# Kernel optimization log

Hardware: AMD Instinct MI355X
Metric: run time of the kernel (lower is better)

The kernel has to match this reference:

```python
import jax, jax.numpy as jnp
import numpy as np

H_SIZE = 1024
N_HEADS = 16
D_K = H_SIZE // N_HEADS


def setup_inputs() -> dict:
    key = jax.random.key(0)
    ks = jax.random.split(key, 12)
    s = 1.0 / np.sqrt(H_SIZE)
    inp = {
        "x": jax.random.normal(ks[0], (2, 2048, H_SIZE), dtype=jnp.float32),
        "Wq": jax.random.uniform(ks[1], (H_SIZE, H_SIZE), minval=-s, maxval=s),
        "bq": jax.random.uniform(ks[2], (H_SIZE,), minval=-s, maxval=s),
        "Wk": jax.random.uniform(ks[3], (H_SIZE, H_SIZE), minval=-s, maxval=s),
        "bk": jax.random.uniform(ks[4], (H_SIZE,), minval=-s, maxval=s),
        "Wv": jax.random.uniform(ks[5], (H_SIZE, H_SIZE), minval=-s, maxval=s),
        "bv": jax.random.uniform(ks[6], (H_SIZE,), minval=-s, maxval=s),
        "Wo": jax.random.uniform(ks[7], (H_SIZE, H_SIZE), minval=-s, maxval=s),
        "bo": jax.random.uniform(ks[8], (H_SIZE,), minval=-s, maxval=s),
        "ln_gamma": jnp.ones((H_SIZE,), dtype=jnp.float32),
        "ln_beta": jnp.zeros((H_SIZE,), dtype=jnp.float32),
    }
    return inp


def reference(x, Wq, bq, Wk, bk, Wv, bv, Wo, bo, ln_gamma, ln_beta):
    B, L, H = x.shape
    residual = x
    # QKV projections -> [B, n_heads, L, d_k]
    def proj(W, b):
        return (x @ W.T + b).reshape(B, L, N_HEADS, D_K).transpose(0, 2, 1, 3)
    q = proj(Wq, bq)
    k = proj(Wk, bk)
    v = proj(Wv, bv)
    # scaled dot-product attention (dropout = identity in eval mode)
    scores = jnp.einsum("bhqd,bhkd->bhqk", q, k) / jnp.sqrt(jnp.float32(D_K))
    attn = jax.nn.softmax(scores, axis=-1)
    out = jnp.einsum("bhqk,bhkd->bhqd", attn, v)
    out = out.transpose(0, 2, 1, 3).reshape(B, L, H)
    out = out @ Wo.T + bo
    # residual + LayerNorm
    y = out + residual
    mu = jnp.mean(y, axis=-1, keepdims=True)
    var = jnp.var(y, axis=-1, keepdims=True)
    y = (y - mu) / jnp.sqrt(var + 1e-5) * ln_gamma + ln_beta
    return y
```

## Files before the change

kernel.cpp:

```cpp
#include <hip/hip_runtime.h>

#define H_SIZE 1024
#define N_HEADS 16
#define D_K 64
#define SEQ 2048
#define BATCH 2
#define M_TOT 4096

typedef __bf16 __attribute__((ext_vector_type(8))) bf16_8;
typedef float __attribute__((ext_vector_type(4))) f32x4;
typedef float __attribute__((ext_vector_type(16))) f32x16;
typedef int __attribute__((ext_vector_type(4))) int4v;

__device__ __forceinline__ ushort f2bf(float f) {
    unsigned int u = __float_as_uint(f);
    unsigned int r = (u + 0x7FFFu + ((u >> 16) & 1u)) >> 16;
    return (ushort)r;
}

__device__ __forceinline__ unsigned int cvtpk(float lo, float hi) {
    unsigned int r;
    asm("v_cvt_pk_bf16_f32 %0, %1, %2" : "=v"(r) : "v"(lo), "v"(hi));
    return r;
}

__device__ __forceinline__ void gld16(void* lds, const void* g) {
    __builtin_amdgcn_global_load_lds(
        (const __attribute__((address_space(1))) unsigned int*)g,
        (__attribute__((address_space(3))) unsigned int*)lds, 16, 0, 0);
}

__global__ __launch_bounds__(256) void cast_all_kernel(
    const float* __restrict__ x, const float* __restrict__ wq, const float* __restrict__ wk,
    const float* __restrict__ wv, const float* __restrict__ wo,
    ushort* __restrict__ xb, ushort* __restrict__ wqb, ushort* __restrict__ wkb,
    ushort* __restrict__ wvb, ushort* __restrict__ wob) {
    int i = blockIdx.x * 256 + threadIdx.x;
    const float* src;
    ushort* dst;
    int off;
    if (i < 1048576) {
        src = x; dst = xb; off = i;
    } else {
        int j = i - 1048576;
        int w = j >> 18;
        off = j & 262143;
        src = (w == 0) ? wq : (w == 1) ? wk : (w == 2) ? wv : wo;
        dst = (w == 0) ? wqb : (w == 1) ? wkb : (w == 2) ? wvb : wob;
    }
    float4 v = ((const float4*)src)[off];
    ushort4 o;
    o.x = f2bf(v.x); o.y = f2bf(v.y); o.z = f2bf(v.z); o.w = f2bf(v.w);
    ((ushort4*)dst)[off] = o;
}

__global__ __launch_bounds__(256) void gemm_qkv(
    const ushort* __restrict__ A, const ushort* __restrict__ wq,
    const ushort* __restrict__ wk, const ushort* __restrict__ wv,
    const float* __restrict__ bq, const float* __restrict__ bk, const float* __restrict__ bv,
    ushort* __restrict__ Qb, ushort* __restrict__ Kb, ushort* __restrict__ Vtb) {
    constexpr int BK = 64, LDST = 72;
    __shared__ ushort As[128 * LDST];
    __shared__ ushort Bs[128 * LDST];
    const int tid = threadIdx.x;
    const int lane = tid & 63, wid = tid >> 6;
    const int wr = wid >> 1, wc = wid & 1;
    const int hi = lane >> 4, lo = lane & 15;
    const int bm0 = blockIdx.x * 128;
    const int t3 = blockIdx.y >> 3;
    const int bn0 = (blockIdx.y & 7) * 128;
    const ushort* Bw = (t3 == 0) ? wq : (t3 == 1) ? wk : wv;
    const float* bias = (t3 == 0) ? bq : (t3 == 1) ? bk : bv;
    ushort* outp = (t3 == 0) ? Qb : (t3 == 1) ? Kb : Vtb;

    f32x4 acc[4][4] = {};

    const int r = tid >> 1, seg = (tid & 1) * 32;
    const ushort* ga = A + (size_t)(bm0 + r) * H_SIZE + seg;
    const ushort* gb = Bw + (size_t)(bn0 + r) * H_SIZE + seg;
    ushort* sa = As + r * LDST + seg;
    ushort* sb = Bs + r * LDST + seg;

    for (int kt = 0; kt < H_SIZE; kt += BK) {
        int4v a0 = *(const int4v*)(ga);
        int4v a1 = *(const int4v*)(ga + 8);
        int4v a2 = *(const int4v*)(ga + 16);
        int4v a3 = *(const int4v*)(ga + 24);
        int4v b0 = *(const int4v*)(gb);
        int4v b1 = *(const int4v*)(gb + 8);
        int4v b2 = *(const int4v*)(gb + 16);
        int4v b3 = *(const int4v*)(gb + 24);
        ga += BK; gb += BK;
        __syncthreads();
        *(int4v*)(sa) = a0; *(int4v*)(sa + 8) = a1;
        *(int4v*)(sa + 16) = a2; *(int4v*)(sa + 24) = a3;
        *(int4v*)(sb) = b0; *(int4v*)(sb + 8) = b1;
        *(int4v*)(sb + 16) = b2; *(int4v*)(sb + 24) = b3;
        __syncthreads();
#pragma unroll
        for (int kk = 0; kk < BK; kk += 32) {
            bf16_8 af[4], bfr[4];
            const ushort* pa = As + (wr * 64 + lo) * LDST + kk + hi * 8;
            const ushort* pb = Bs + (wc * 64 + lo) * LDST + kk + hi * 8;
#pragma unroll
            for (int i = 0; i < 4; i++) af[i] = *(const bf16_8*)(pa + i * 16 * LDST);
#pragma unroll
            for (int i = 0; i < 4; i++) bfr[i] = *(const bf16_8*)(pb + i * 16 * LDST);
#pragma unroll
            for (int mi = 0; mi < 4; mi++)
#pragma unroll
                for (int ni = 0; ni < 4; ni++)
                    acc[mi][ni] = __builtin_amdgcn_mfma_f32_16x16x32_bf16(
                        af[mi], bfr[ni], acc[mi][ni], 0, 0, 0);
        }
    }

#pragma unroll
    for (int mi = 0; mi < 4; mi++) {
#pragma unroll
        for (int ni = 0; ni < 4; ni++) {
            const int row0 = bm0 + wr * 64 + mi * 16 + hi * 4;
            const int col = bn0 + wc * 64 + ni * 16 + lo;
            const float bv = bias[col];
            const int h = col >> 6, dk = col & 63;
#pragma unroll
            for (int rr = 0; rr < 4; rr++) {
                const int m = row0 + rr;
                const int b = m >> 11, l = m & 2047;
                float val = acc[mi][ni][rr] + bv;
                if (t3 == 0) {
                    outp[((size_t)(b * N_HEADS + h) * SEQ + l) * D_K + dk] = f2bf(val * 0.125f);
                } else if (t3 == 1) {
                    int dks = (((dk >> 3) ^ (l & 7)) << 3) | (dk & 7);
                    outp[((size_t)(b * N_HEADS + h) * SEQ + l) * D_K + dks] = f2bf(val);
                } else {
                    int lsw = (l & ~63) | ((((l >> 3) & 7) ^ (dk & 7)) << 3) | (l & 7);
                    outp[((size_t)(b * N_HEADS + h) * D_K + dk) * SEQ + lsw] = f2bf(val);
                }
            }
        }
    }
}

__global__ __launch_bounds__(256) void gemm_o(const ushort* __restrict__ A,
                                              const ushort* __restrict__ Bw,
                                              const float* __restrict__ bias,
                                              const float* __restrict__ resid,
                                              float* __restrict__ outp) {
    constexpr int BK = 64, LDST = 72;
    __shared__ ushort As[128 * LDST];
    __shared__ ushort Bs[64 * LDST];
    const int tid = threadIdx.x;
    const int lane = tid & 63, wid = tid >> 6;
    const int wr = wid >> 1, wc = wid & 1;
    const int hi = lane >> 4, lo = lane & 15;
    const int bm0 = blockIdx.x * 128, bn0 = blockIdx.y * 64;

    f32x4 acc[4][2] = {};

    const int ra = tid >> 1, sega = (tid & 1) * 32;
    const int rb = tid >> 2, segb = (tid & 3) * 16;
    const ushort* ga = A + (size_t)(bm0 + ra) * H_SIZE + sega;
    const ushort* gb = Bw + (size_t)(bn0 + rb) * H_SIZE + segb;
    ushort* sa = As + ra * LDST + sega;
    ushort* sb = Bs + rb * LDST + segb;

    for (int kt = 0; kt < H_SIZE; kt += BK) {
        int4v a0 = *(const int4v*)(ga);
        int4v a1 = *(const int4v*)(ga + 8);
        int4v a2 = *(const int4v*)(ga + 16);
        int4v a3 = *(const int4v*)(ga + 24);
        int4v b0 = *(const int4v*)(gb);
        int4v b1 = *(const int4v*)(gb + 8);
        ga += BK; gb += BK;
        __syncthreads();
        *(int4v*)(sa) = a0; *(int4v*)(sa + 8) = a1;
        *(int4v*)(sa + 16) = a2; *(int4v*)(sa + 24) = a3;
        *(int4v*)(sb) = b0; *(int4v*)(sb + 8) = b1;
        __syncthreads();
#pragma unroll
        for (int kk = 0; kk < BK; kk += 32) {
            bf16_8 af[4], bfr[2];
            const ushort* pa = As + (wr * 64 + lo) * LDST + kk + hi * 8;
            const ushort* pb = Bs + (wc * 32 + lo) * LDST + kk + hi * 8;
#pragma unroll
            for (int i = 0; i < 4; i++) af[i] = *(const bf16_8*)(pa + i * 16 * LDST);
#pragma unroll
            for (int i = 0; i < 2; i++) bfr[i] = *(const bf16_8*)(pb + i * 16 * LDST);
#pragma unroll
            for (int mi = 0; mi < 4; mi++)
#pragma unroll
                for (int ni = 0; ni < 2; ni++)
                    acc[mi][ni] = __builtin_amdgcn_mfma_f32_16x16x32_bf16(
                        af[mi], bfr[ni], acc[mi][ni], 0, 0, 0);
        }
    }

#pragma unroll
    for (int mi = 0; mi < 4; mi++) {
#pragma unroll
        for (int ni = 0; ni < 2; ni++) {
            const int row0 = bm0 + wr * 64 + mi * 16 + hi * 4;
            const int col = bn0 + wc * 32 + ni * 16 + lo;
            const float bv = bias[col];
#pragma unroll
            for (int rr = 0; rr < 4; rr++) {
                const int m = row0 + rr;
                outp[(size_t)m * H_SIZE + col] =
                    acc[mi][ni][rr] + bv + resid[(size_t)m * H_SIZE + col];
            }
        }
    }
}

__global__ __launch_bounds__(256) void attn_kernel(const ushort* __restrict__ Q,
                                                   const ushort* __restrict__ Ksw,
                                                   const ushort* __restrict__ Vsw,
                                                   ushort* __restrict__ Out) {
    __shared__ ushort Ks[2][64 * 64];
    __shared__ ushort Vs[2][64 * 64];
    __shared__ float lsum_lds[4][32];
    const int lane = threadIdx.x & 63, wid = threadIdx.x >> 6;
    const int h32 = lane >> 5, q32 = lane & 31;
    const int bh = blockIdx.y;
    const int q0w = blockIdx.x * 128 + wid * 32;
    const ushort* Qh = Q + (size_t)bh * SEQ * D_K;
    const ushort* Kp = Ksw + (size_t)bh * SEQ * D_K;
    const ushort* Vp = Vsw + (size_t)bh * D_K * SEQ;

    bf16_8 qf[4];
#pragma unroll
    for (int tt = 0; tt < 4; tt++)
        qf[tt] = *(const bf16_8*)(Qh + (size_t)(q0w + q32) * D_K + tt * 16 + h32 * 8);

    f32x16 oacc0 = {}, oacc1 = {};
    float ls = 0.f;

    const int koff = wid * 2048 + lane * 16;
    const int vrow = wid * 16 + (lane >> 3);
    const int vseg = (lane & 7) * 16;

#define STAGE(bb, kt)                                                             \
    {                                                                             \
        const char* kg = (const char*)(Kp + (size_t)(kt) * D_K);                  \
        char* kl = (char*)&Ks[bb][0];                                             \
        gld16(kl + koff, kg + koff);                                              \
        gld16(kl + koff + 1024, kg + koff + 1024);                                \
        char* vl = (char*)&Vs[bb][0];                                             \
        gld16(vl + vrow * 128 + vseg,                                             \
              (const char*)(Vp + (size_t)vrow * SEQ + (kt)) + vseg);              \
        gld16(vl + (vrow + 8) * 128 + vseg,                                       \
              (const char*)(Vp + (size_t)(vrow + 8) * SEQ + (kt)) + vseg);        \
    }

    STAGE(0, 0);
    __syncthreads();
    int buf = 0;
    for (int t = 0; t < SEQ / 64; t++) {
        if (t + 1 < SEQ / 64) STAGE(buf ^ 1, (t + 1) * 64);
        const ushort* kb = &Ks[buf][0];
        const ushort* vb = &Vs[buf][0];
#pragma unroll
        for (int kh = 0; kh < 2; kh++) {
            f32x16 st = {};
            const int krow = kh * 32 + q32;
#pragma unroll
            for (int tt = 0; tt < 4; tt++) {
                int sg = ((2 * tt + h32) ^ (krow & 7));
                bf16_8 kf = *(const bf16_8*)(kb + krow * 64 + sg * 8);
                st = __builtin_amdgcn_mfma_f32_32x32x16_bf16(kf, qf[tt], st, 0, 0, 0);
            }
            float p[16];
#pragma unroll
            for (int rr = 0; rr < 16; rr++) p[rr] = __expf(st[rr]);
            float partial = 0.f;
#pragma unroll
            for (int rr = 0; rr < 16; rr++) partial += p[rr];
            ls += partial + __shfl_xor(partial, 32);

            union { unsigned int w[4]; bf16_8 v; } pf0, pf1;
#pragma unroll
            for (int i = 0; i < 2; i++) {
                unsigned int a = cvtpk(p[2 * i], p[2 * i + 1]);
                unsigned int b = cvtpk(p[4 + 2 * i], p[4 + 2 * i + 1]);
                asm volatile("v_permlane32_swap_b32 %0, %1" : "+v"(a), "+v"(b));
                pf0.w[i] = a; pf0.w[2 + i] = b;
                unsigned int c = cvtpk(p[8 + 2 * i], p[8 + 2 * i + 1]);
                unsigned int d = cvtpk(p[12 + 2 * i], p[12 + 2 * i + 1]);
                asm volatile("v_permlane32_swap_b32 %0, %1" : "+v"(c), "+v"(d));
                pf1.w[i] = c; pf1.w[2 + i] = d;
            }

            {
                const int vr0 = q32;
                int sg0 = ((4 * kh + h32) ^ (vr0 & 7));
                int sg1 = ((4 * kh + 2 + h32) ^ (vr0 & 7));
                bf16_8 vf0 = *(const bf16_8*)(vb + vr0 * 64 + sg0 * 8);
                bf16_8 vf1 = *(const bf16_8*)(vb + vr0 * 64 + sg1 * 8);
                oacc0 = __builtin_amdgcn_mfma_f32_32x32x16_bf16(pf0.v, vf0, oacc0, 0, 0, 0);
                oacc0 = __builtin_amdgcn_mfma_f32_32x32x16_bf16(pf1.v, vf1, oacc0, 0, 0, 0);
            }
            {
                const int vr1 = 32 + q32;
                int sg0 = ((4 * kh + h32) ^ (vr1 & 7));
                int sg1 = ((4 * kh + 2 + h32) ^ (vr1 & 7));
                bf16_8 vf0 = *(const bf16_8*)(vb + vr1 * 64 + sg0 * 8);
                bf16_8 vf1 = *(const bf16_8*)(vb + vr1 * 64 + sg1 * 8);
                oacc1 = __builtin_amdgcn_mfma_f32_32x32x16_bf16(pf0.v, vf0, oacc1, 0, 0, 0);
                oacc1 = __builtin_amdgcn_mfma_f32_32x32x16_bf16(pf1.v, vf1, oacc1, 0, 0, 0);
            }
        }
        __syncthreads();
        buf ^= 1;
    }
#undef STAGE

    if (lane < 32) lsum_lds[wid][q32] = 1.0f / ls;
    const int b = bh >> 4, h = bh & 15;
#pragma unroll
    for (int rr = 0; rr < 16; rr++) {
        const int qloc = (rr & 3) + 8 * (rr >> 2) + 4 * h32;
        const float inv = lsum_lds[wid][qloc];
        const int l = q0w + qloc;
        ushort* orow = Out + ((size_t)(b * SEQ + l)) * H_SIZE + h * 64;
        orow[q32] = f2bf(oacc0[rr] * inv);
        orow[32 + q32] = f2bf(oacc1[rr] * inv);
    }
}

__global__ __launch_bounds__(256) void ln_kernel(float* __restrict__ y,
                                                 const float* __restrict__ gamma,
                                                 const float* __restrict__ beta) {
    const int row = blockIdx.x;
    float4* p = (float4*)(y + (size_t)row * H_SIZE);
    float4 v = p[threadIdx.x];
    float s = v.x + v.y + v.z + v.w;
    float s2 = v.x * v.x + v.y * v.y + v.z * v.z + v.w * v.w;
#pragma unroll
    for (int off = 1; off < 64; off <<= 1) {
        s += __shfl_xor(s, off);
        s2 += __shfl_xor(s2, off);
    }
    __shared__ float ss[4], ss2[4];
    const int wid = threadIdx.x >> 6, lane = threadIdx.x & 63;
    if (lane == 0) { ss[wid] = s; ss2[wid] = s2; }
    __syncthreads();
    s = ss[0] + ss[1] + ss[2] + ss[3];
    s2 = ss2[0] + ss2[1] + ss2[2] + ss2[3];
    const float mean = s * (1.0f / H_SIZE);
    const float var = s2 * (1.0f / H_SIZE) - mean * mean;
    const float rstd = rsqrtf(var + 1e-5f);
    const float4 g = ((const float4*)gamma)[threadIdx.x];
    const float4 bt = ((const float4*)beta)[threadIdx.x];
    float4 o;
    o.x = (v.x - mean) * rstd * g.x + bt.x;
    o.y = (v.y - mean) * rstd * g.y + bt.y;
    o.z = (v.z - mean) * rstd * g.z + bt.z;
    o.w = (v.w - mean) * rstd * g.w + bt.w;
    p[threadIdx.x] = o;
}

extern "C" void kernel_launch(void* const* d_in, const int* in_sizes, int n_in,
                              void* d_out, int out_size, void* d_ws, size_t ws_size,
                              hipStream_t stream) {
    const float* x = (const float*)d_in[0];
    const float* Wq = (const float*)d_in[1];
    const float* bq = (const float*)d_in[2];
    const float* Wk = (const float*)d_in[3];
    const float* bk = (const float*)d_in[4];
    const float* Wv = (const float*)d_in[5];
    const float* bv = (const float*)d_in[6];
    const float* Wo = (const float*)d_in[7];
    const float* bo = (const float*)d_in[8];
    const float* gamma = (const float*)d_in[9];
    const float* beta = (const float*)d_in[10];

    char* ws = (char*)d_ws;
    ushort* xb  = (ushort*)(ws);
    ushort* wqb = (ushort*)(ws + (8u << 20));
    ushort* wkb = (ushort*)(ws + (10u << 20));
    ushort* wvb = (ushort*)(ws + (12u << 20));
    ushort* wob = (ushort*)(ws + (14u << 20));
    ushort* Qb  = (ushort*)(ws + (16u << 20));
    ushort* Kb  = (ushort*)(ws + (24u << 20));
    ushort* Vtb = (ushort*)(ws + (32u << 20));
    ushort* Ao  = (ushort*)(ws + (40u << 20));

    cast_all_kernel<<<8192, 256, 0, stream>>>(x, Wq, Wk, Wv, Wo, xb, wqb, wkb, wvb, wob);

    dim3 gq(M_TOT / 128, 24);
    gemm_qkv<<<gq, 256, 0, stream>>>(xb, wqb, wkb, wvb, bq, bk, bv, Qb, Kb, Vtb);

    dim3 g2(SEQ / 128, BATCH * N_HEADS);
    attn_kernel<<<g2, 256, 0, stream>>>(Qb, Kb, Vtb, Ao);

    dim3 go(M_TOT / 128, H_SIZE / 64);
    gemm_o<<<go, 256, 0, stream>>>(Ao, wob, bo, x, (float*)d_out);

    ln_kernel<<<M_TOT, 256, 0, stream>>>((float*)d_out, gamma, beta);
}
```

Measured before the change: 141.8 us.

## Double-buffer LDS in QKV and output GEMMs and vectorize V-transpose stores

Both projection GEMMs switch from single-buffered BK=64 tiles with two barriers per step to double-buffered BK=32 tiles. The next tile's global loads are issued before the MFMAs on the current tile, and only one barrier is needed per step. The V output, written transposed, now packs the four consecutive rows of each accumulator into a single ushort4 store instead of four scalar stores. The cost is twice as many loop iterations with less MFMA work each, which may leave less compute to hide latency between barriers.

```diff
diff --git a/kernel.cpp b/kernel.cpp
--- a/kernel.cpp
+++ b/kernel.cpp
@@ -59,9 +59,9 @@
     const ushort* __restrict__ wk, const ushort* __restrict__ wv,
     const float* __restrict__ bq, const float* __restrict__ bk, const float* __restrict__ bv,
     ushort* __restrict__ Qb, ushort* __restrict__ Kb, ushort* __restrict__ Vtb) {
-    constexpr int BK = 64, LDST = 72;
-    __shared__ ushort As[128 * LDST];
-    __shared__ ushort Bs[128 * LDST];
+    constexpr int LDST = 40;
+    __shared__ ushort As[2][128 * LDST];
+    __shared__ ushort Bs[2][128 * LDST];
     const int tid = threadIdx.x;
     const int lane = tid & 63, wid = tid >> 6;
     const int wr = wid >> 1, wc = wid & 1;
@@ -71,49 +71,59 @@
     const int bn0 = (blockIdx.y & 7) * 128;
     const ushort* Bw = (t3 == 0) ? wq : (t3 == 1) ? wk : wv;
     const float* bias = (t3 == 0) ? bq : (t3 == 1) ? bk : bv;
-    ushort* outp = (t3 == 0) ? Qb : (t3 == 1) ? Kb : Vtb;
 
     f32x4 acc[4][4] = {};
 
-    const int r = tid >> 1, seg = (tid & 1) * 32;
-    const ushort* ga = A + (size_t)(bm0 + r) * H_SIZE + seg;
-    const ushort* gb = Bw + (size_t)(bn0 + r) * H_SIZE + seg;
-    ushort* sa = As + r * LDST + seg;
-    ushort* sb = Bs + r * LDST + seg;
-
-    for (int kt = 0; kt < H_SIZE; kt += BK) {
-        int4v a0 = *(const int4v*)(ga);
-        int4v a1 = *(const int4v*)(ga + 8);
-        int4v a2 = *(const int4v*)(ga + 16);
-        int4v a3 = *(const int4v*)(ga + 24);
-        int4v b0 = *(const int4v*)(gb);
-        int4v b1 = *(const int4v*)(gb + 8);
-        int4v b2 = *(const int4v*)(gb + 16);
-        int4v b3 = *(const int4v*)(gb + 24);
-        ga += BK; gb += BK;
-        __syncthreads();
-        *(int4v*)(sa) = a0; *(int4v*)(sa + 8) = a1;
-        *(int4v*)(sa + 16) = a2; *(int4v*)(sa + 24) = a3;
-        *(int4v*)(sb) = b0; *(int4v*)(sb + 8) = b1;
-        *(int4v*)(sb + 16) = b2; *(int4v*)(sb + 24) = b3;
-        __syncthreads();
-#pragma unroll
-        for (int kk = 0; kk < BK; kk += 32) {
-            bf16_8 af[4], bfr[4];
-            const ushort* pa = As + (wr * 64 + lo) * LDST + kk + hi * 8;
-            const ushort* pb = Bs + (wc * 64 + lo) * LDST + kk + hi * 8;
+    const int r = tid >> 1, c0 = (tid & 1) * 16;
+    const ushort* ga = A + (size_t)(bm0 + r) * H_SIZE + c0;
+    const ushort* gb = Bw + (size_t)(bn0 + r) * H_SIZE + c0;
+
+    int4v a0, a1, b0, b1;
+#define LOADR(kt)                                  \
+    {                                              \
+        a0 = *(const int4v*)(ga + (kt));           \
+        a1 = *(const int4v*)(ga + (kt) + 8);       \
+        b0 = *(const int4v*)(gb + (kt));           \
+        b1 = *(const int4v*)(gb + (kt) + 8);       \
+    }
+#define STORER(bb)                                 \
+    {                                              \
+        ushort* sa = &As[bb][r * LDST + c0];       \
+        *(int4v*)sa = a0; *(int4v*)(sa + 8) = a1;  \
+        ushort* sb = &Bs[bb][r * LDST + c0];       \
+        *(int4v*)sb = b0; *(int4v*)(sb + 8) = b1;  \
+    }
+
+    LOADR(0);
+    STORER(0);
+    __syncthreads();
+    int cur = 0;
+    constexpr int NT = H_SIZE / 32;
+    for (int t = 0; t < NT; t++) {
+        if (t + 1 < NT) LOADR((t + 1) * 32);
+        {
+            bf16_8 af[4], bfv[4];
+            const ushort* pa = &As[cur][(wr * 64 + lo) * LDST + hi * 8];
+            const ushort* pb = &Bs[cur][(wc * 64 + lo) * LDST + hi * 8];
 #pragma unroll
             for (int i = 0; i < 4; i++) af[i] = *(const bf16_8*)(pa + i * 16 * LDST);
 #pragma unroll
-            for (int i = 0; i < 4; i++) bfr[i] = *(const bf16_8*)(pb + i * 16 * LDST);
+            for (int i = 0; i < 4; i++) bfv[i] = *(const bf16_8*)(pb + i * 16 * LDST);
 #pragma unroll
             for (int mi = 0; mi < 4; mi++)
 #pragma unroll
                 for (int ni = 0; ni < 4; ni++)
                     acc[mi][ni] = __builtin_amdgcn_mfma_f32_16x16x32_bf16(
-                        af[mi], bfr[ni], acc[mi][ni], 0, 0, 0);
-        }
-    }
+                        af[mi], bfv[ni], acc[mi][ni], 0, 0, 0);
+        }
+        if (t + 1 < NT) {
+            STORER(cur ^ 1);
+            __syncthreads();
+        }
+        cur ^= 1;
+    }
+#undef LOADR
+#undef STORER
 
 #pragma unroll
     for (int mi = 0; mi < 4; mi++) {
@@ -123,19 +133,27 @@
             const int col = bn0 + wc * 64 + ni * 16 + lo;
             const float bv = bias[col];
             const int h = col >> 6, dk = col & 63;
-#pragma unroll
-            for (int rr = 0; rr < 4; rr++) {
-                const int m = row0 + rr;
-                const int b = m >> 11, l = m & 2047;
-                float val = acc[mi][ni][rr] + bv;
-                if (t3 == 0) {
-                    outp[((size_t)(b * N_HEADS + h) * SEQ + l) * D_K + dk] = f2bf(val * 0.125f);
-                } else if (t3 == 1) {
-                    int dks = (((dk >> 3) ^ (l & 7)) << 3) | (dk & 7);
-                    outp[((size_t)(b * N_HEADS + h) * SEQ + l) * D_K + dks] = f2bf(val);
-                } else {
-                    int lsw = (l & ~63) | ((((l >> 3) & 7) ^ (dk & 7)) << 3) | (l & 7);
-                    outp[((size_t)(b * N_HEADS + h) * D_K + dk) * SEQ + lsw] = f2bf(val);
+            if (t3 == 2) {
+                const int b = row0 >> 11, l0 = row0 & 2047;
+                const int lsw0 = (l0 & ~63) | ((((l0 >> 3) & 7) ^ (dk & 7)) << 3) | (l0 & 7);
+                ushort4 o;
+                o.x = f2bf(acc[mi][ni][0] + bv);
+                o.y = f2bf(acc[mi][ni][1] + bv);
+                o.z = f2bf(acc[mi][ni][2] + bv);
+                o.w = f2bf(acc[mi][ni][3] + bv);
+                *(ushort4*)&Vtb[((size_t)(b * N_HEADS + h) * D_K + dk) * SEQ + lsw0] = o;
+            } else {
+#pragma unroll
+                for (int rr = 0; rr < 4; rr++) {
+                    const int m = row0 + rr;
+                    const int b = m >> 11, l = m & 2047;
+                    float val = acc[mi][ni][rr] + bv;
+                    if (t3 == 0) {
+                        Qb[((size_t)(b * N_HEADS + h) * SEQ + l) * D_K + dk] = f2bf(val * 0.125f);
+                    } else {
+                        int dks = (((dk >> 3) ^ (l & 7)) << 3) | (dk & 7);
+                        Kb[((size_t)(b * N_HEADS + h) * SEQ + l) * D_K + dks] = f2bf(val);
+                    }
                 }
             }
         }
@@ -147,9 +165,9 @@
                                               const float* __restrict__ bias,
                                               const float* __restrict__ resid,
                                               float* __restrict__ outp) {
-    constexpr int BK = 64, LDST = 72;
-    __shared__ ushort As[128 * LDST];
-    __shared__ ushort Bs[64 * LDST];
+    constexpr int LDST = 40;
+    __shared__ ushort As[2][128 * LDST];
+    __shared__ ushort Bs[2][64 * LDST];
     const int tid = threadIdx.x;
     const int lane = tid & 63, wid = tid >> 6;
     const int wr = wid >> 1, wc = wid & 1;
@@ -158,43 +176,55 @@
 
     f32x4 acc[4][2] = {};
 
-    const int ra = tid >> 1, sega = (tid & 1) * 32;
-    const int rb = tid >> 2, segb = (tid & 3) * 16;
-    const ushort* ga = A + (size_t)(bm0 + ra) * H_SIZE + sega;
-    const ushort* gb = Bw + (size_t)(bn0 + rb) * H_SIZE + segb;
-    ushort* sa = As + ra * LDST + sega;
-    ushort* sb = Bs + rb * LDST + segb;
-
-    for (int kt = 0; kt < H_SIZE; kt += BK) {
-        int4v a0 = *(const int4v*)(ga);
-        int4v a1 = *(const int4v*)(ga + 8);
-        int4v a2 = *(const int4v*)(ga + 16);
-        int4v a3 = *(const int4v*)(ga + 24);
-        int4v b0 = *(const int4v*)(gb);
-        int4v b1 = *(const int4v*)(gb + 8);
-        ga += BK; gb += BK;
-        __syncthreads();
-        *(int4v*)(sa) = a0; *(int4v*)(sa + 8) = a1;
-        *(int4v*)(sa + 16) = a2; *(int4v*)(sa + 24) = a3;
-        *(int4v*)(sb) = b0; *(int4v*)(sb + 8) = b1;
-        __syncthreads();
-#pragma unroll
-        for (int kk = 0; kk < BK; kk += 32) {
-            bf16_8 af[4], bfr[2];
-            const ushort* pa = As + (wr * 64 + lo) * LDST + kk + hi * 8;
-            const ushort* pb = Bs + (wc * 32 + lo) * LDST + kk + hi * 8;
+    const int ra = tid >> 1, ca0 = (tid & 1) * 16;
+    const int rb = tid >> 2, cb0 = (tid & 3) * 8;
+    const ushort* ga = A + (size_t)(bm0 + ra) * H_SIZE + ca0;
+    const ushort* gb = Bw + (size_t)(bn0 + rb) * H_SIZE + cb0;
+
+    int4v a0, a1, b0;
+#define LOADR(kt)                                  \
+    {                                              \
+        a0 = *(const int4v*)(ga + (kt));           \
+        a1 = *(const int4v*)(ga + (kt) + 8);       \
+        b0 = *(const int4v*)(gb + (kt));           \
+    }
+#define STORER(bb)                                 \
+    {                                              \
+        ushort* sa = &As[bb][ra * LDST + ca0];     \
+        *(int4v*)sa = a0; *(int4v*)(sa + 8) = a1;  \
+        *(int4v*)&Bs[bb][rb * LDST + cb0] = b0;    \
+    }
+
+    LOADR(0);
+    STORER(0);
+    __syncthreads();
+    int cur = 0;
+    constexpr int NT = H_SIZE / 32;
+    for (int t = 0; t < NT; t++) {
+        if (t + 1 < NT) LOADR((t + 1) * 32);
+        {
+            bf16_8 af[4], bfv[2];
+            const ushort* pa = &As[cur][(wr * 64 + lo) * LDST + hi * 8];
+            const ushort* pb = &Bs[cur][(wc * 32 + lo) * LDST + hi * 8];
 #pragma unroll
             for (int i = 0; i < 4; i++) af[i] = *(const bf16_8*)(pa + i * 16 * LDST);
 #pragma unroll
-            for (int i = 0; i < 2; i++) bfr[i] = *(const bf16_8*)(pb + i * 16 * LDST);
+            for (int i = 0; i < 2; i++) bfv[i] = *(const bf16_8*)(pb + i * 16 * LDST);
 #pragma unroll
             for (int mi = 0; mi < 4; mi++)
 #pragma unroll
                 for (int ni = 0; ni < 2; ni++)
                     acc[mi][ni] = __builtin_amdgcn_mfma_f32_16x16x32_bf16(
-                        af[mi], bfr[ni], acc[mi][ni], 0, 0, 0);
-        }
-    }
+                        af[mi], bfv[ni], acc[mi][ni], 0, 0, 0);
+        }
+        if (t + 1 < NT) {
+            STORER(cur ^ 1);
+            __syncthreads();
+        }
+        cur ^= 1;
+    }
+#undef LOADR
+#undef STORER
 
 #pragma unroll
     for (int mi = 0; mi < 4; mi++) {
```

After: 135.6 us. 4.4% less time.
